# Performance work log

Hardware: AMD Instinct MI355X
Metric: run time of the kernel (lower is better)

The kernel has to match this reference:

```python
import jax, jax.numpy as jnp
import numpy as np

POOLED_H = 7
POOLED_W = 7
SPATIAL_SCALE = 0.25
SAMPLING = 2  # bilinear samples per bin edge (standard Mask R-CNN setting)


def setup_inputs() -> dict:
    key = jax.random.key(0)
    k1, k2, k3, k4 = jax.random.split(key, 4)
    B, C, H, W = 2, 256, 200, 304
    K = 1024
    IMG_H, IMG_W = 800.0, 1216.0  # input-image coords; feature map = img * spatial_scale
    features = jax.random.normal(k1, (B, C, H, W), dtype=jnp.float32)
    bidx = jax.random.randint(k2, (K,), 0, B).astype(jnp.float32)
    xs = jnp.sort(jax.random.uniform(k3, (K, 2), dtype=jnp.float32) * IMG_W, axis=1)
    ys = jnp.sort(jax.random.uniform(k4, (K, 2), dtype=jnp.float32) * IMG_H, axis=1)
    rois = jnp.stack([bidx, xs[:, 0], ys[:, 0], xs[:, 1], ys[:, 1]], axis=1)  # [K,5]
    return {"features": features, "rois": rois}


def _axis_interp(coord, size):
    # coord: [K, S] continuous sample positions along one axis of length `size`.
    # Returns low/high integer indices and bilinear weights (zeroed outside [-1, size]).
    valid = ((coord >= -1.0) & (coord <= jnp.float32(size))).astype(coord.dtype)
    c = jnp.clip(coord, 0.0, jnp.float32(size - 1))
    lo = jnp.floor(c)
    hi = jnp.minimum(lo + 1.0, jnp.float32(size - 1))
    frac = c - lo
    return lo.astype(jnp.int32), hi.astype(jnp.int32), (1.0 - frac) * valid, frac * valid


def reference(features, rois):
    B, C, H, W = features.shape
    K = rois.shape[0]
    bidx = rois[:, 0].astype(jnp.int32)
    x1 = rois[:, 1] * SPATIAL_SCALE
    y1 = rois[:, 2] * SPATIAL_SCALE
    x2 = rois[:, 3] * SPATIAL_SCALE
    y2 = rois[:, 4] * SPATIAL_SCALE
    roi_w = jnp.maximum(x2 - x1, 1.0)
    roi_h = jnp.maximum(y2 - y1, 1.0)
    bin_w = roi_w / POOLED_W
    bin_h = roi_h / POOLED_H

    # sample coords: y = y1 + ((j + 0.5)/S) * bin_h, j = py*S + iy  -> [K, PH*S]
    jy = (jnp.arange(POOLED_H * SAMPLING, dtype=jnp.float32) + 0.5) / SAMPLING
    jx = (jnp.arange(POOLED_W * SAMPLING, dtype=jnp.float32) + 0.5) / SAMPLING
    ys = y1[:, None] + jy[None, :] * bin_h[:, None]  # [K, Ys]
    xs = x1[:, None] + jx[None, :] * bin_w[:, None]  # [K, Xs]

    ylo, yhi, wy0, wy1 = _axis_interp(ys, H)
    xlo, xhi, wx0, wx1 = _axis_interp(xs, W)

    b = bidx[:, None, None]  # [K,1,1]

    def gather(yi, xi):
        # advanced indexing -> [K, Ys, Xs, C]
        return features[b, :, yi[:, :, None], xi[:, None, :]]

    def wgt(wy, wx):
        return (wy[:, :, None] * wx[:, None, :])[..., None]  # [K,Ys,Xs,1]

    v = (gather(ylo, xlo) * wgt(wy0, wx0)
         + gather(ylo, xhi) * wgt(wy0, wx1)
         + gather(yhi, xlo) * wgt(wy1, wx0)
         + gather(yhi, xhi) * wgt(wy1, wx1))  # [K, Ys, Xs, C]

    # average the SxS samples within each bin
    v = v.reshape(K, POOLED_H, SAMPLING, POOLED_W, SAMPLING, C).mean(axis=(2, 4))
    return jnp.transpose(v, (0, 3, 1, 2))  # [K, C, PH, PW]
```

## Files before the change

### kernel.cpp

```cpp
#include <hip/hip_runtime.h>
#include <hip/hip_fp16.h>

#define CC 256
#define HH 200
#define WW 304
#define PHW 49
#define XT 16
#define NCHUNK 2
#define CHC 128
#define SSTR 132

struct Interp { int lo, hi; float w0, w1; };

__device__ __forceinline__ Interp axis_interp(float coord, int size) {
  float valid = (coord >= -1.0f && coord <= (float)size) ? 1.0f : 0.0f;
  float c = fminf(fmaxf(coord, 0.0f), (float)(size - 1));
  float fl = floorf(c);
  int lo = (int)fl;
  int hi = min(lo + 1, size - 1);
  float fr = c - fl;
  Interp r;
  r.lo = lo; r.hi = hi;
  r.w0 = (1.0f - fr) * valid;
  r.w1 = fr * valid;
  return r;
}

__device__ __forceinline__ float4 h4_to_f4(ushort4 u) {
  __half2 a = *(__half2*)&u.x;
  __half2 b = *(__half2*)&u.z;
  float2 fa = __half22float2(a);
  float2 fb = __half22float2(b);
  return make_float4(fa.x, fa.y, fb.x, fb.y);
}

__global__ __launch_bounds__(1024) void k_sortrois(const float* __restrict__ rois,
                                                   int K, int Bp,
                                                   int* __restrict__ perm) {
  __shared__ int whist[16][32];
  __shared__ int keytot[32];
  __shared__ int keybase[32];
  int tid = threadIdx.x;
  if (K > 1024) {
    for (int i = tid; i < K; i += 1024) perm[i] = i;
    return;
  }
  int wave = tid >> 6, lane = tid & 63;
  bool active = tid < K;
  int key = 63;
  if (active) {
    const float* r = rois + (size_t)tid * 5;
    int b = (int)r[0];
    float cx = (r[1] + r[3]) * 0.125f;
    float cy = (r[2] + r[4]) * 0.125f;
    int rx = (int)(cx * (8.0f / (float)WW)); rx = max(0, min(7, rx));
    int ry = cy >= (float)(HH / 2) ? 1 : 0;
    key = (((b & 1) * 2 + ry) * 8 + rx) & 31;
  }
  if (tid < 512) ((int*)whist)[tid] = 0;
  __syncthreads();
  unsigned long long m = ~0ull;
#pragma unroll
  for (int bit = 0; bit < 6; ++bit) {
    unsigned long long bb = __ballot((key >> bit) & 1);
    m &= ((key >> bit) & 1) ? bb : ~bb;
  }
  unsigned long long below = m & ((1ull << lane) - 1ull);
  int rank = __popcll(below);
  if (active && below == 0ull) whist[wave][key] = __popcll(m);
  __syncthreads();
  if (tid < 32) {
    int total = 0;
    for (int w = 0; w < 16; ++w) {
      int t = whist[w][tid];
      whist[w][tid] = total;
      total += t;
    }
    keytot[tid] = total;
  }
  __syncthreads();
  if (tid == 0) {
    int base = 0;
    for (int k2 = 0; k2 < 32; ++k2) { keybase[k2] = base; base += keytot[k2]; }
  }
  __syncthreads();
  if (active) perm[keybase[key] + whist[wave][key] + rank] = tid;
}

__global__ __launch_bounds__(256) void k_transpose_f16c(const float* __restrict__ src,
                                                        __half* __restrict__ dst,
                                                        int Bp) {
  __shared__ float tile[XT][CC + 4];
  int plane = blockIdx.y;
  int x0 = blockIdx.x * XT;
  int b = plane / HH;
  int y = plane - b * HH;
  const float* sp = src + (size_t)b * CC * HH * WW + (size_t)y * WW + x0;
  int cr = threadIdx.x >> 2;
  int x4 = (threadIdx.x & 3) * 4;
#pragma unroll
  for (int pass = 0; pass < 4; ++pass) {
    int c = cr + pass * 64;
    float4 v = *(const float4*)(sp + (size_t)c * HH * WW + x4);
    tile[x4 + 0][c] = v.x;
    tile[x4 + 1][c] = v.y;
    tile[x4 + 2][c] = v.z;
    tile[x4 + 3][c] = v.w;
  }
  __syncthreads();
  int xw = threadIdx.x >> 5;
  int co = (threadIdx.x & 31) * 8;
  int chunk = co >> 7;
  int cc = co & 127;
#pragma unroll
  for (int pass = 0; pass < 2; ++pass) {
    int x = xw + pass * 8;
    const float* trow = &tile[x][co];
    union { uint4 u; __half2 h[4]; } pk;
    pk.h[0] = __floats2half2_rn(trow[0], trow[1]);
    pk.h[1] = __floats2half2_rn(trow[2], trow[3]);
    pk.h[2] = __floats2half2_rn(trow[4], trow[5]);
    pk.h[3] = __floats2half2_rn(trow[6], trow[7]);
    size_t idx = (((size_t)chunk * Bp + b) * (size_t)(HH * WW) +
                  (size_t)y * WW + (x0 + x)) * CHC + cc;
    *(uint4*)(dst + idx) = pk.u;
  }
}

__global__ __launch_bounds__(512, 8) void k_gather(const __half* __restrict__ feat,
                                                   const float* __restrict__ rois,
                                                   const int* __restrict__ perm,
                                                   float* __restrict__ out,
                                                   int K, int Bp) {
  __shared__ float stage[PHW][SSTR];
  __shared__ int   xoff[14][2];
  __shared__ float xwgt[14][2];
  __shared__ int2  yoff[14];
  __shared__ float2 ywgt[14];
  int q = gridDim.x >> 3;
  int bx = blockIdx.x;
  int slot = (bx & 7) * q + (bx >> 3);
  if (slot >= K) return;
  int k = perm[slot];
  int chunk = blockIdx.y;

  const float* r = rois + (size_t)k * 5;
  int b = __builtin_amdgcn_readfirstlane((int)r[0]);
  float x1 = r[1] * 0.25f, y1 = r[2] * 0.25f;
  float x2 = r[3] * 0.25f, y2 = r[4] * 0.25f;
  float bin_w = fmaxf(x2 - x1, 1.0f) * (1.0f / 7.0f);
  float bin_h = fmaxf(y2 - y1, 1.0f) * (1.0f / 7.0f);

  int tid = threadIdx.x;
  if (tid < 32) {
    int axis = tid >> 4;
    int j = tid & 15;
    if (j < 14) {
      float start = axis ? y1 : x1;
      float binsz = axis ? bin_h : bin_w;
      int size = axis ? HH : WW;
      float coord = start + ((float)j + 0.5f) * 0.5f * binsz;
      Interp ii = axis_interp(coord, size);
      if (axis) {
        yoff[j] = make_int2(ii.lo * (WW * CHC * 2), ii.hi * (WW * CHC * 2));
        ywgt[j] = make_float2(ii.w0, ii.w1);
      } else {
        xoff[j][0] = ii.lo * (CHC * 2);
        xoff[j][1] = ii.hi * (CHC * 2);
        xwgt[j][0] = ii.w0 * 0.25f;
        xwgt[j][1] = ii.w1 * 0.25f;
      }
    }
  }
  __syncthreads();

  int wave = tid >> 6;
  int lane = tid & 63;
  int xsel = lane >> 5;
  int cq = lane & 31;
  const char* fb = (const char*)(feat +
      ((size_t)chunk * Bp + b) * (size_t)(HH * WW) * CHC);
  int laneByte = cq * 8;

  for (int p = wave; p < PHW; p += 8) {
    int ph = p / 7;
    int pw = p - ph * 7;
    int jx0 = 2 * pw, jy0 = 2 * ph;
    int2 yo0 = yoff[jy0], yo1 = yoff[jy0 + 1];
    float2 yw0 = ywgt[jy0], yw1 = ywgt[jy0 + 1];
    __half2 w00 = __float2half2_rn(yw0.x), w01 = __float2half2_rn(yw0.y);
    __half2 w10 = __float2half2_rn(yw1.x), w11 = __float2half2_rn(yw1.y);
    float ax = 0.f, ay = 0.f, az = 0.f, aw = 0.f;
#pragma unroll
    for (int sx = 0; sx < 2; ++sx) {
      int xo = xoff[jx0 + sx][xsel] + laneByte;
      float wx = xwgt[jx0 + sx][xsel];
#pragma unroll
      for (int sy = 0; sy < 2; ++sy) {
        const __half2 wlo = sy ? w10 : w00;
        const __half2 whi = sy ? w11 : w01;
        int2 yo = sy ? yo1 : yo0;
        ushort4 u0 = *(const ushort4*)(fb + (yo.x + xo));
        ushort4 u1 = *(const ushort4*)(fb + (yo.y + xo));
        __half2 t0 = __hfma2(*(__half2*)&u1.x, whi, __hmul2(*(__half2*)&u0.x, wlo));
        __half2 t1 = __hfma2(*(__half2*)&u1.z, whi, __hmul2(*(__half2*)&u0.z, wlo));
        float2 f0 = __half22float2(t0);
        float2 f1 = __half22float2(t1);
        ax += wx * f0.x; ay += wx * f0.y;
        az += wx * f1.x; aw += wx * f1.y;
      }
    }
    ax += __shfl_xor(ax, 32);
    ay += __shfl_xor(ay, 32);
    az += __shfl_xor(az, 32);
    aw += __shfl_xor(aw, 32);
    if (lane < 32) {
      float* s = &stage[p][cq * 4];
      s[0] = ax; s[1] = ay; s[2] = az; s[3] = aw;
    }
  }
  __syncthreads();

  float* outk = out + (size_t)k * CC * PHW + (size_t)chunk * CHC * PHW;
  for (int i = tid; i < CHC * PHW; i += 512) {
    int cc = i / PHW;
    int p = i - cc * PHW;
    outk[i] = stage[p][cc];
  }
}

__global__ __launch_bounds__(256) void k_roialign_direct(const float* __restrict__ fe,
                                                         const float* __restrict__ rois,
                                                         float* __restrict__ out,
                                                         int total) {
  int idx = blockIdx.x * 256 + threadIdx.x;
  if (idx >= total) return;
  int pw = idx % 7;
  int t = idx / 7;
  int ph = t % 7; t /= 7;
  int c = t % CC;
  int k = t / CC;
  const float* r = rois + (size_t)k * 5;
  int b = (int)r[0];
  float x1 = r[1] * 0.25f, y1 = r[2] * 0.25f;
  float x2 = r[3] * 0.25f, y2 = r[4] * 0.25f;
  float bin_w = fmaxf(x2 - x1, 1.0f) * (1.0f / 7.0f);
  float bin_h = fmaxf(y2 - y1, 1.0f) * (1.0f / 7.0f);
  const float* base = fe + ((size_t)b * CC + c) * HH * WW;
  float acc = 0.f;
#pragma unroll
  for (int sy = 0; sy < 2; ++sy) {
    float yy = y1 + ((float)(2 * ph + sy) + 0.5f) * 0.5f * bin_h;
    Interp iy = axis_interp(yy, HH);
#pragma unroll
    for (int sx = 0; sx < 2; ++sx) {
      float xx = x1 + ((float)(2 * pw + sx) + 0.5f) * 0.5f * bin_w;
      Interp ix = axis_interp(xx, WW);
      float v00 = base[(size_t)iy.lo * WW + ix.lo];
      float v01 = base[(size_t)iy.lo * WW + ix.hi];
      float v10 = base[(size_t)iy.hi * WW + ix.lo];
      float v11 = base[(size_t)iy.hi * WW + ix.hi];
      acc += iy.w0 * ix.w0 * v00 + iy.w0 * ix.w1 * v01 +
             iy.w1 * ix.w0 * v10 + iy.w1 * ix.w1 * v11;
    }
  }
  out[idx] = acc * 0.25f;
}

extern "C" void kernel_launch(void* const* d_in, const int* in_sizes, int n_in,
                              void* d_out, int out_size, void* d_ws, size_t ws_size,
                              hipStream_t stream) {
  const float* features = (const float*)d_in[0];
  const float* rois = (const float*)d_in[1];
  float* out = (float*)d_out;
  int B = in_sizes[0] / (CC * HH * WW);
  int K = in_sizes[1] / 5;
  size_t feat_bytes = (size_t)B * HH * WW * CC * sizeof(__half);
  size_t perm_bytes = (size_t)((K + 7) & ~7) * sizeof(int);
  if (ws_size >= feat_bytes + perm_bytes && K <= 1024) {
    __half* feat16 = (__half*)d_ws;
    int* perm = (int*)((char*)d_ws + feat_bytes);
    k_sortrois<<<1, 1024, 0, stream>>>(rois, K, B, perm);
    dim3 tg(WW / XT, B * HH);
    k_transpose_f16c<<<tg, 256, 0, stream>>>(features, feat16, B);
    int q = (K + 7) / 8;
    dim3 gg(8 * q, NCHUNK);
    k_gather<<<gg, 512, 0, stream>>>(feat16, rois, perm, out, K, B);
  } else {
    int total = K * CC * PHW;
    k_roialign_direct<<<(total + 255) / 256, 256, 0, stream>>>(features, rois, out, total);
  }
}
```

Baseline: 91.38 us.

## Fuse transpose and gather into one persistent cooperative kernel with grid sync

Replaces the separate transpose and gather launches with one cooperative kernel of 1024 persistent blocks. Each block first converts feature tiles to a chunked fp16 channel-last layout, then all blocks meet at a grid-wide barrier before doing the ROI gather, which now multiplies in half precision. The aim is to remove one kernel launch and the gap between launches. In exchange it adds a grid sync, lower occupancy constraints from launch bounds, and host-side occupancy queries on every call. It falls back to the old path if cooperative launch is unavailable.

```diff
diff --git a/kernel.cpp b/kernel.cpp
--- a/kernel.cpp
+++ b/kernel.cpp
@@ -1,5 +1,8 @@
 #include <hip/hip_runtime.h>
 #include <hip/hip_fp16.h>
+#include <hip/hip_cooperative_groups.h>
+
+namespace cg = cooperative_groups;
 
 #define CC 256
 #define HH 200
@@ -9,6 +12,8 @@
 #define NCHUNK 2
 #define CHC 128
 #define SSTR 132
+#define SSTR2 133
+#define GBLK 1024
 
 struct Interp { int lo, hi; float w0, w1; };
 
@@ -85,6 +90,158 @@
   }
   __syncthreads();
   if (active) perm[keybase[key] + whist[wave][key] + rank] = tid;
+}
+
+__global__ __launch_bounds__(512, 8) void k_fused(const float* __restrict__ src,
+                                                  __half* __restrict__ feat,
+                                                  const float* __restrict__ rois,
+                                                  const int* __restrict__ perm,
+                                                  float* __restrict__ out,
+                                                  int K, int Bp) {
+  __shared__ float shbuf[PHW * SSTR2];
+  __shared__ int   xoff[14][2];
+  __shared__ float xwgt[14][2];
+  __shared__ int2  yoff[14];
+  __shared__ float2 ywgt[14];
+
+  int tid = threadIdx.x;
+  int bid = blockIdx.x;
+
+  {
+    float (*tile)[CC + 4] = (float (*)[CC + 4])shbuf;
+    int ntx = WW / XT;
+    int nTiles = ntx * (Bp * HH);
+    int cr = tid >> 2;
+    int x4 = (tid & 3) * 4;
+    int xw = tid >> 5;
+    int co = (tid & 31) * 8;
+    int chunk = co >> 7;
+    int cc = co & 127;
+    for (int t = bid; t < nTiles; t += GBLK) {
+      int xt = t % ntx;
+      int plane = t / ntx;
+      int b = plane / HH;
+      int y = plane - b * HH;
+      int x0 = xt * XT;
+      const float* sp = src + (size_t)b * CC * HH * WW + (size_t)y * WW + x0;
+      __syncthreads();
+#pragma unroll
+      for (int pass = 0; pass < 2; ++pass) {
+        int c = cr + pass * 128;
+        float4 v = *(const float4*)(sp + (size_t)c * HH * WW + x4);
+        tile[x4 + 0][c] = v.x;
+        tile[x4 + 1][c] = v.y;
+        tile[x4 + 2][c] = v.z;
+        tile[x4 + 3][c] = v.w;
+      }
+      __syncthreads();
+      const float* trow = &tile[xw][co];
+      union { int4 i4; __half2 h[4]; } pk;
+      pk.h[0] = __floats2half2_rn(trow[0], trow[1]);
+      pk.h[1] = __floats2half2_rn(trow[2], trow[3]);
+      pk.h[2] = __floats2half2_rn(trow[4], trow[5]);
+      pk.h[3] = __floats2half2_rn(trow[6], trow[7]);
+      size_t idx = (((size_t)chunk * Bp + b) * (size_t)(HH * WW) +
+                    (size_t)y * WW + (x0 + xw)) * CHC + cc;
+      *(int4*)(feat + idx) = pk.i4;
+    }
+  }
+  cg::this_grid().sync();
+
+  {
+    float (*stage)[SSTR2] = (float (*)[SSTR2])shbuf;
+    int q = (K + 7) / 8;
+    int pairsPerChunk = 8 * q;
+    int nPairs = NCHUNK * pairsPerChunk;
+    int lane = tid & 63;
+    int wave = tid >> 6;
+    int xsel = (lane >> 4) & 1;
+    int ysel = lane >> 5;
+    int cq = lane & 15;
+    int cqByte = cq * 16;
+
+    for (int pair = bid; pair < nPairs; pair += GBLK) {
+      int chunk = pair / pairsPerChunk;
+      int si = pair - chunk * pairsPerChunk;
+      int slot = (si & 7) * q + (si >> 3);
+      __syncthreads();
+      if (slot >= K) continue;
+      int k = perm[slot];
+      const float* r = rois + (size_t)k * 5;
+      int b = __builtin_amdgcn_readfirstlane((int)r[0]);
+      float x1 = r[1] * 0.25f, y1 = r[2] * 0.25f;
+      float x2 = r[3] * 0.25f, y2 = r[4] * 0.25f;
+      float bin_w = fmaxf(x2 - x1, 1.0f) * (1.0f / 7.0f);
+      float bin_h = fmaxf(y2 - y1, 1.0f) * (1.0f / 7.0f);
+      if (tid < 32) {
+        int axis = tid >> 4;
+        int j = tid & 15;
+        if (j < 14) {
+          float start = axis ? y1 : x1;
+          float binsz = axis ? bin_h : bin_w;
+          int size = axis ? HH : WW;
+          float coord = start + ((float)j + 0.5f) * 0.5f * binsz;
+          Interp ii = axis_interp(coord, size);
+          if (axis) {
+            yoff[j] = make_int2(ii.lo * (WW * CHC * 2), ii.hi * (WW * CHC * 2));
+            ywgt[j] = make_float2(ii.w0, ii.w1);
+          } else {
+            xoff[j][0] = ii.lo * (CHC * 2);
+            xoff[j][1] = ii.hi * (CHC * 2);
+            xwgt[j][0] = ii.w0 * 0.25f;
+            xwgt[j][1] = ii.w1 * 0.25f;
+          }
+        }
+      }
+      __syncthreads();
+
+      const char* fb = (const char*)feat +
+          ((size_t)chunk * Bp + b) * (size_t)(HH * WW) * (CHC * 2);
+
+      for (int p = wave; p < PHW; p += 8) {
+        int ph = p / 7;
+        int pw = p - ph * 7;
+        int jx0 = 2 * pw, jy0 = 2 * ph;
+        float acc[8] = {0.f, 0.f, 0.f, 0.f, 0.f, 0.f, 0.f, 0.f};
+#pragma unroll
+        for (int s = 0; s < 4; ++s) {
+          int jx = jx0 + (s & 1);
+          int jy = jy0 + (s >> 1);
+          int xo = xoff[jx][xsel];
+          int2 yy = yoff[jy];
+          int yo = ysel ? yy.y : yy.x;
+          float2 yw = ywgt[jy];
+          float w = xwgt[jx][xsel] * (ysel ? yw.y : yw.x);
+          union { int4 i4; __half2 h[4]; } u;
+          u.i4 = *(const int4*)(fb + ((size_t)(yo + xo) + cqByte));
+          __half2 wh = __float2half2_rn(w);
+#pragma unroll
+          for (int i = 0; i < 4; ++i) {
+            float2 f = __half22float2(__hmul2(u.h[i], wh));
+            acc[2 * i] += f.x;
+            acc[2 * i + 1] += f.y;
+          }
+        }
+#pragma unroll
+        for (int i = 0; i < 8; ++i) acc[i] += __shfl_xor(acc[i], 16);
+#pragma unroll
+        for (int i = 0; i < 8; ++i) acc[i] += __shfl_xor(acc[i], 32);
+        if (lane < 16) {
+          float* sdst = &stage[p][cq * 8];
+#pragma unroll
+          for (int i = 0; i < 8; ++i) sdst[i] = acc[i];
+        }
+      }
+      __syncthreads();
+
+      float* outk = out + (size_t)k * CC * PHW + (size_t)chunk * CHC * PHW;
+      for (int i = tid; i < CHC * PHW; i += 512) {
+        int cc2 = i / PHW;
+        int p = i - cc2 * PHW;
+        outk[i] = stage[p][cc2];
+      }
+    }
+  }
 }
 
 __global__ __launch_bounds__(256) void k_transpose_f16c(const float* __restrict__ src,
@@ -277,15 +434,31 @@
   int K = in_sizes[1] / 5;
   size_t feat_bytes = (size_t)B * HH * WW * CC * sizeof(__half);
   size_t perm_bytes = (size_t)((K + 7) & ~7) * sizeof(int);
+
   if (ws_size >= feat_bytes + perm_bytes && K <= 1024) {
     __half* feat16 = (__half*)d_ws;
     int* perm = (int*)((char*)d_ws + feat_bytes);
+
+    int maxPerCU = 0, coopAttr = 0, numCU = 0;
+    hipError_t e1 = hipOccupancyMaxActiveBlocksPerMultiprocessor(
+        &maxPerCU, k_fused, 512, 0);
+    (void)hipDeviceGetAttribute(&coopAttr, hipDeviceAttributeCooperativeLaunch, 0);
+    (void)hipDeviceGetAttribute(&numCU, hipDeviceAttributeMultiprocessorCount, 0);
+    bool coop_ok = (e1 == hipSuccess) && coopAttr && (maxPerCU * numCU >= GBLK);
+
     k_sortrois<<<1, 1024, 0, stream>>>(rois, K, B, perm);
-    dim3 tg(WW / XT, B * HH);
-    k_transpose_f16c<<<tg, 256, 0, stream>>>(features, feat16, B);
-    int q = (K + 7) / 8;
-    dim3 gg(8 * q, NCHUNK);
-    k_gather<<<gg, 512, 0, stream>>>(feat16, rois, perm, out, K, B);
+    if (coop_ok) {
+      void* args[] = {(void*)&features, (void*)&feat16, (void*)&rois,
+                      (void*)&perm, (void*)&out, (void*)&K, (void*)&B};
+      (void)hipLaunchCooperativeKernel((void*)k_fused, dim3(GBLK), dim3(512),
+                                       args, 0, stream);
+    } else {
+      dim3 tg(WW / XT, B * HH);
+      k_transpose_f16c<<<tg, 256, 0, stream>>>(features, feat16, B);
+      int q = (K + 7) / 8;
+      dim3 gg(8 * q, NCHUNK);
+      k_gather<<<gg, 512, 0, stream>>>(feat16, rois, perm, out, K, B);
+    }
   } else {
     int total = K * CC * PHW;
     k_roialign_direct<<<(total + 255) / 256, 256, 0, stream>>>(features, rois, out, total);
```

Measured after the change: 91.73 us. Within noise of the previous version (+0.4%).
